# Kernel optimization log

Measured on AMD Instinct MI355X. Metric: run time of the kernel, lower is better.

## Reference

```python
import jax, jax.numpy as jnp
import numpy as np
import math

D = 1024      # d_model
H = 4096      # expert hidden
E = 8         # num_experts
K = 2         # top_k
CAP_FACTOR = 1.25
B, S = 4, 2048
T = B * S
CAP = int(math.ceil(CAP_FACTOR * T * K / E))  # 2560


def setup_inputs() -> dict:
    key = jax.random.key(0)
    ks = jax.random.split(key, 6)
    x  = jax.random.normal(ks[0], (B, S, D), dtype=jnp.float32)
    Wr = jax.random.normal(ks[1], (D, E), dtype=jnp.float32) * (1.0 / np.sqrt(D))
    W1 = jax.random.normal(ks[2], (E, D, H), dtype=jnp.float32) * (1.0 / np.sqrt(D))
    b1 = jnp.zeros((E, H), dtype=jnp.float32)
    W2 = jax.random.normal(ks[3], (E, H, D), dtype=jnp.float32) * (1.0 / np.sqrt(H))
    b2 = jnp.zeros((E, D), dtype=jnp.float32)
    return {"x": x, "Wr": Wr, "W1": W1, "b1": b1, "W2": W2, "b2": b2}


def reference(x, Wr, W1, b1, W2, b2):
    x_flat = x.reshape(T, D)

    # ---- Router: top-k softmax gating (temp = 1.0), renormalized weights ----
    logits = jnp.einsum('td,de->te', x_flat, Wr)
    probs = jax.nn.softmax(logits, axis=-1)
    topk_w, topk_idx = jax.lax.top_k(probs, K)            # [T,K]
    topk_w = topk_w / jnp.sum(topk_w, axis=-1, keepdims=True)

    # ---- Vectorized capacity-based dispatch ----
    e = topk_idx.reshape(-1)                               # [T*K] expert id per pair
    onehot = jax.nn.one_hot(e, E, dtype=jnp.int32)         # [T*K, E]
    pos_all = jnp.cumsum(onehot, axis=0) - 1               # slot within expert
    pos = jnp.take_along_axis(pos_all, e[:, None], axis=1)[:, 0]
    keep = pos < CAP
    # dropped pairs go to a dummy slot E*CAP (sliced off / zero-padded)
    dest = jnp.where(keep, e * CAP + pos, E * CAP)         # [T*K]

    x_pairs = jnp.repeat(x_flat, K, axis=0)                # [T*K, D]
    buf = jnp.zeros((E * CAP + 1, D), dtype=x.dtype).at[dest].set(x_pairs)
    expert_in = buf[:E * CAP].reshape(E, CAP, D)

    # ---- Grouped expert MLP (GELU) ----
    h = jax.nn.gelu(jnp.einsum('ecd,edh->ech', expert_in, W1) + b1[:, None, :])
    expert_out = jnp.einsum('ech,ehd->ecd', h, W2) + b2[:, None, :]

    # ---- Combine: gather back and weight; dropped tokens get zeros ----
    out_pad = jnp.concatenate(
        [expert_out.reshape(E * CAP, D), jnp.zeros((1, D), dtype=x.dtype)], axis=0)
    y_pairs = out_pad[dest] * topk_w.reshape(-1)[:, None]  # [T*K, D]
    y_flat = y_pairs.reshape(T, K, D).sum(axis=1)
    return y_flat.reshape(B, S, D)
```

## Files before the change

### kernel.cpp

```cpp
#include <hip/hip_runtime.h>
#include <stdint.h>

#define D_MODEL 1024
#define H_DIM   4096
#define NE      8
#define NCAP    2560
#define NTOK    8192
#define NPAIR   (NTOK * 2)

typedef __attribute__((ext_vector_type(8))) __bf16 bf16x8;
typedef __attribute__((ext_vector_type(4))) float  f32x4;
typedef __attribute__((ext_vector_type(8))) unsigned short ushort8;

__device__ __forceinline__ unsigned short f2bf(float f) {
  union { float f; unsigned u; } v; v.f = f;
  unsigned r = v.u + 0x7fffu + ((v.u >> 16) & 1u);
  return (unsigned short)(r >> 16);
}
__device__ __forceinline__ float bf2f(unsigned short s) {
  union { unsigned u; float f; } v; v.u = ((unsigned)s) << 16;
  return v.f;
}
__device__ __forceinline__ float gelu_tanh(float x) {
  float u = 0.7978845608028654f * (x + 0.044715f * x * x * x);
  float e = __expf(2.0f * u);
  float th = 1.0f - 2.0f / (e + 1.0f);
  return 0.5f * x * (1.0f + th);
}
__device__ __forceinline__ void load_lds16(const void* g, void* l) {
  __builtin_amdgcn_global_load_lds(
      (const __attribute__((address_space(1))) unsigned int*)g,
      (__attribute__((address_space(3))) unsigned int*)l, 16, 0, 0);
}

__global__ __launch_bounds__(256) void router_kernel(
    const float* __restrict__ x, const float* __restrict__ Wr,
    int* __restrict__ pair_e, float* __restrict__ pair_w) {
  int lane = threadIdx.x & 63;
  int t = blockIdx.x * 4 + (threadIdx.x >> 6);
  float acc[NE];
#pragma unroll
  for (int e = 0; e < NE; ++e) acc[e] = 0.0f;
  const float* xr = x + (size_t)t * D_MODEL;
  for (int d = lane; d < D_MODEL; d += 64) {
    float xv = xr[d];
#pragma unroll
    for (int e = 0; e < NE; ++e) acc[e] = fmaf(xv, Wr[d * NE + e], acc[e]);
  }
#pragma unroll
  for (int off = 32; off > 0; off >>= 1) {
#pragma unroll
    for (int e = 0; e < NE; ++e) acc[e] += __shfl_down(acc[e], off, 64);
  }
  if (lane == 0) {
    int i1 = 0;
#pragma unroll
    for (int e = 1; e < NE; ++e) if (acc[e] > acc[i1]) i1 = e;
    int i2 = (i1 == 0) ? 1 : 0;
#pragma unroll
    for (int e = 0; e < NE; ++e) if (e != i1 && acc[e] > acc[i2]) i2 = e;
    float p2 = expf(acc[i2] - acc[i1]);
    float inv = 1.0f / (1.0f + p2);
    pair_e[t * 2]     = i1;  pair_e[t * 2 + 1] = i2;
    pair_w[t * 2]     = inv;
    pair_w[t * 2 + 1] = p2 * inv;
  }
}

__global__ __launch_bounds__(1024) void assign_kernel(
    const int* __restrict__ pair_e, int* __restrict__ pair_dest,
    int* __restrict__ counts) {
  __shared__ int wtot[16][NE];
  const int tid = threadIdx.x;
  const int lane = tid & 63, w = tid >> 6;

  int ids[16];
  const int4* pe = (const int4*)(pair_e + tid * 16);
#pragma unroll
  for (int q = 0; q < 4; ++q) {
    int4 v = pe[q];
    ids[q * 4 + 0] = v.x; ids[q * 4 + 1] = v.y;
    ids[q * 4 + 2] = v.z; ids[q * 4 + 3] = v.w;
  }
  int c[NE];
#pragma unroll
  for (int e = 0; e < NE; ++e) c[e] = 0;
#pragma unroll
  for (int j = 0; j < 16; ++j) c[ids[j]]++;

  int incl[NE];
#pragma unroll
  for (int e = 0; e < NE; ++e) incl[e] = c[e];
#pragma unroll
  for (int d = 1; d < 64; d <<= 1) {
#pragma unroll
    for (int e = 0; e < NE; ++e) {
      int u = __shfl_up(incl[e], d, 64);
      if (lane >= d) incl[e] += u;
    }
  }
  if (lane == 63) {
#pragma unroll
    for (int e = 0; e < NE; ++e) wtot[w][e] = incl[e];
  }
  __syncthreads();
  if (tid < NE) {
    int run = 0;
#pragma unroll
    for (int ww = 0; ww < 16; ++ww) {
      int t2 = wtot[ww][tid];
      wtot[ww][tid] = run;
      run += t2;
    }
    counts[tid] = run < NCAP ? run : NCAP;
  }
  __syncthreads();

  int off[NE];
#pragma unroll
  for (int e = 0; e < NE; ++e) off[e] = wtot[w][e] + incl[e] - c[e];
#pragma unroll
  for (int j = 0; j < 16; ++j) {
    int e = ids[j];
    int pos = off[e]++;
    pair_dest[tid * 16 + j] = (pos < NCAP) ? (e * NCAP + pos) : (NE * NCAP);
  }
}

__global__ __launch_bounds__(64) void dispatch_kernel(
    const float* __restrict__ x, const int* __restrict__ pair_dest,
    unsigned short* __restrict__ Xd) {
  int i = blockIdx.x;
  int dest = pair_dest[i];
  if (dest >= NE * NCAP) return;
  int lane = threadIdx.x;
  int t = i >> 1;
  const float4* xr = (const float4*)(x + (size_t)t * D_MODEL);
  ushort4* dr = (ushort4*)(Xd + (size_t)dest * D_MODEL);
#pragma unroll
  for (int c = 0; c < 4; ++c) {
    float4 v = xr[lane + c * 64];
    ushort4 o;
    o.x = f2bf(v.x); o.y = f2bf(v.y); o.z = f2bf(v.z); o.w = f2bf(v.w);
    dr[lane + c * 64] = o;
  }
}

__global__ __launch_bounds__(256) void transpose_cvt(
    const float* __restrict__ src, unsigned short* __restrict__ dst,
    int R, int C) {
  __shared__ float tile[64][69];
  int e = blockIdx.z;
  int c0 = blockIdx.x * 64, r0 = blockIdx.y * 64;
  const float* s = src + (size_t)e * R * C + (size_t)r0 * C + c0;
  int tc = (threadIdx.x & 15) * 4;
  int tr = threadIdx.x >> 4;
#pragma unroll
  for (int it = 0; it < 4; ++it) {
    int row = tr + it * 16;
    float4 v = *(const float4*)(s + (size_t)row * C + tc);
    tile[row][tc]     = v.x; tile[row][tc + 1] = v.y;
    tile[row][tc + 2] = v.z; tile[row][tc + 3] = v.w;
  }
  __syncthreads();
  unsigned short* d = dst + (size_t)e * R * C + (size_t)c0 * R + r0;
  int oc  = threadIdx.x >> 3;
  int orr = (threadIdx.x & 7) * 8;
#pragma unroll
  for (int it = 0; it < 2; ++it) {
    int crow = oc + it * 32;
    ushort8 v;
#pragma unroll
    for (int j = 0; j < 8; ++j) v[j] = f2bf(tile[orr + j][crow]);
    *(ushort8*)(d + (size_t)crow * R + orr) = v;
  }
}

__global__ __launch_bounds__(512, 2) void moe_gemm_pipe(
    const unsigned short* __restrict__ Abase,
    const unsigned short* __restrict__ Bbase,
    const float* __restrict__ bias,
    unsigned short* __restrict__ Cout,
    const int* __restrict__ counts,
    int N, int K, int NX, int do_gelu) {
  const int M = NCAP;
  const int KT = K >> 6;
  __shared__ char smem[131072];

  int orig = blockIdx.x;
  int q = (NX * NE) >> 3;
  int wgid = (orig & 7) * q + (orig >> 3);
  const int e = wgid / NX;
  int r = wgid % NX;

  int grp = r >> 2, lid = r & 3;
  int gm = grp % 5, gn = grp / 5;
  const int m0 = (gm * 2 + (lid & 1)) * 256;
  const int n0 = (gn * 2 + (lid >> 1)) * 256;
  if (m0 >= counts[e]) return;

  const int tid = threadIdx.x;
  const int lane = tid & 63;
  const int wid = tid >> 6;
  const int wm = (wid >> 2) * 128;
  const int wn = (wid & 3) * 64;

  const unsigned short* A = Abase + (size_t)e * M * K;
  const unsigned short* B = Bbase + (size_t)e * N * K;

  f32x4 acc[8][4];
  f32x4 zero = {0.f, 0.f, 0.f, 0.f};
#pragma unroll
  for (int i = 0; i < 8; ++i)
#pragma unroll
    for (int j = 0; j < 4; ++j) acc[i][j] = zero;

  const unsigned short* ga[4];
  const unsigned short* gb[4];
  int ldso[4];
#pragma unroll
  for (int c = 0; c < 4; ++c) {
    int ci = c * 512 + tid;
    int row = ci >> 3;
    int sc = (ci & 7) ^ (row & 7);
    ga[c] = A + (size_t)(m0 + row) * K + sc * 8;
    gb[c] = B + (size_t)(n0 + row) * K + sc * 8;
    ldso[c] = (c * 512 + wid * 64) * 16;
  }

#pragma unroll
  for (int c = 0; c < 4; ++c) {
    load_lds16(ga[c], smem + ldso[c]);          ga[c] += 64;
    load_lds16(gb[c], smem + 32768 + ldso[c]);  gb[c] += 64;
  }

  for (int kt = 0; kt < KT; ++kt) {
    __syncthreads();
    const char* Ab = smem + (kt & 1) * 65536;
    const char* Bb = Ab + 32768;
    if (kt + 1 < KT) {
      char* An = smem + ((kt + 1) & 1) * 65536;
#pragma unroll
      for (int c = 0; c < 4; ++c) {
        load_lds16(ga[c], An + ldso[c]);          ga[c] += 64;
        load_lds16(gb[c], An + 32768 + ldso[c]);  gb[c] += 64;
      }
    }
    {
      bf16x8 af[8], bfr[4];
      int lc = (lane >> 4);
#pragma unroll
      for (int f = 0; f < 8; ++f) {
        int ar = wm + f * 16 + (lane & 15);
        af[f] = *(const bf16x8*)(Ab + ar * 128 + ((lc ^ (ar & 7)) * 16));
      }
#pragma unroll
      for (int f = 0; f < 4; ++f) {
        int br = wn + f * 16 + (lane & 15);
        bfr[f] = *(const bf16x8*)(Bb + br * 128 + ((lc ^ (br & 7)) * 16));
      }
      __builtin_amdgcn_s_setprio(1);
#pragma unroll
      for (int i = 0; i < 8; ++i)
#pragma unroll
        for (int j = 0; j < 4; ++j)
          acc[i][j] = __builtin_amdgcn_mfma_f32_16x16x32_bf16(
              af[i], bfr[j], acc[i][j], 0, 0, 0);
      __builtin_amdgcn_s_setprio(0);
    }
    __builtin_amdgcn_s_barrier();
    {
      bf16x8 af[8], bfr[4];
      int lc = 4 + (lane >> 4);
#pragma unroll
      for (int f = 0; f < 8; ++f) {
        int ar = wm + f * 16 + (lane & 15);
        af[f] = *(const bf16x8*)(Ab + ar * 128 + ((lc ^ (ar & 7)) * 16));
      }
#pragma unroll
      for (int f = 0; f < 4; ++f) {
        int br = wn + f * 16 + (lane & 15);
        bfr[f] = *(const bf16x8*)(Bb + br * 128 + ((lc ^ (br & 7)) * 16));
      }
      __builtin_amdgcn_s_setprio(1);
#pragma unroll
      for (int i = 0; i < 8; ++i)
#pragma unroll
        for (int j = 0; j < 4; ++j)
          acc[i][j] = __builtin_amdgcn_mfma_f32_16x16x32_bf16(
              af[i], bfr[j], acc[i][j], 0, 0, 0);
      __builtin_amdgcn_s_setprio(0);
    }
  }

  __syncthreads();
  const float* be = bias + (size_t)e * N;
#pragma unroll
  for (int i = 0; i < 8; ++i) {
    int rbase = wm + i * 16 + ((lane >> 4) << 2);
#pragma unroll
    for (int j = 0; j < 4; ++j) {
      int col = wn + j * 16 + (lane & 15);
      float bv = be[n0 + col];
#pragma unroll
      for (int r2 = 0; r2 < 4; ++r2) {
        float xv = acc[i][j][r2] + bv;
        if (do_gelu) xv = gelu_tanh(xv);
        *(unsigned short*)(smem + (size_t)(rbase + r2) * 512 + col * 2) = f2bf(xv);
      }
    }
  }
  __syncthreads();
#pragma unroll
  for (int it = 0; it < 16; ++it) {
    int idx = it * 4096 + tid * 8;
    int row = idx >> 8, col = idx & 255;
    ushort8 v = *(const ushort8*)(smem + (size_t)idx * 2);
    *(ushort8*)(Cout + ((size_t)e * M + m0 + row) * N + n0 + col) = v;
  }
}

__global__ __launch_bounds__(256) void combine_kernel(
    const unsigned short* __restrict__ Ebuf,
    const int* __restrict__ pair_dest,
    const float* __restrict__ pair_w,
    float* __restrict__ out) {
  int t = blockIdx.x;
  int d0 = threadIdx.x * 4;
  float4 r = {0.f, 0.f, 0.f, 0.f};
#pragma unroll
  for (int k = 0; k < 2; ++k) {
    int dest = pair_dest[t * 2 + k];
    if (dest < NE * NCAP) {
      float w = pair_w[t * 2 + k];
      ushort4 v = *(const ushort4*)(Ebuf + (size_t)dest * D_MODEL + d0);
      r.x += w * bf2f(v.x); r.y += w * bf2f(v.y);
      r.z += w * bf2f(v.z); r.w += w * bf2f(v.w);
    }
  }
  *(float4*)(out + (size_t)t * D_MODEL + d0) = r;
}

extern "C" void kernel_launch(void* const* d_in, const int* in_sizes, int n_in,
                              void* d_out, int out_size, void* d_ws, size_t ws_size,
                              hipStream_t stream) {
  const float* x  = (const float*)d_in[0];
  const float* Wr = (const float*)d_in[1];
  const float* W1 = (const float*)d_in[2];
  const float* b1 = (const float*)d_in[3];
  const float* W2 = (const float*)d_in[4];
  const float* b2 = (const float*)d_in[5];
  float* out = (float*)d_out;

  char* ws = (char*)d_ws;
  unsigned short* W1T  = (unsigned short*)(ws + 0);
  unsigned short* W2T  = (unsigned short*)(ws + 67108864);
  unsigned short* Xd   = (unsigned short*)(ws + 134217728);
  unsigned short* Ebuf = Xd;
  unsigned short* Hbuf = (unsigned short*)(ws + 176160768);
  int*   pair_e    = (int*)(ws + 343932928);
  float* pair_w    = (float*)(ws + 343998464);
  int*   pair_dest = (int*)(ws + 344064000);
  int*   counts    = (int*)(ws + 344129536);

  transpose_cvt<<<dim3(H_DIM / 64, D_MODEL / 64, NE), 256, 0, stream>>>(W1, W1T, D_MODEL, H_DIM);
  transpose_cvt<<<dim3(D_MODEL / 64, H_DIM / 64, NE), 256, 0, stream>>>(W2, W2T, H_DIM, D_MODEL);

  router_kernel<<<NTOK / 4, 256, 0, stream>>>(x, Wr, pair_e, pair_w);
  assign_kernel<<<1, 1024, 0, stream>>>(pair_e, pair_dest, counts);
  dispatch_kernel<<<NPAIR, 64, 0, stream>>>(x, pair_dest, Xd);

  {
    int nx = (NCAP / 256) * (H_DIM / 256);
    moe_gemm_pipe<<<nx * NE, 512, 0, stream>>>(
        Xd, W1T, b1, Hbuf, counts, H_DIM, D_MODEL, nx, 1);
  }
  {
    int nx = (NCAP / 256) * (D_MODEL / 256);
    moe_gemm_pipe<<<nx * NE, 512, 0, stream>>>(
        Hbuf, W2T, b2, Ebuf, counts, D_MODEL, H_DIM, nx, 0);
  }

  combine_kernel<<<NTOK, 256, 0, stream>>>(Ebuf, pair_dest, pair_w, out);
}
```

Measured before the change: 807.3 us.

## Switch expert GEMM to 4-stage K=32 LDS pipeline with explicit vmcnt waits

Restructures the main GEMM loop from a double-buffered K=64 tile into a four-slot ring of K=32 tiles, keeping three tiles of global-to-LDS loads in flight. Each iteration uses a manual s_waitcnt vmcnt count and a single barrier instead of __syncthreads plus two half-steps. A new XOR swizzle fits the 64-byte LDS rows. The goal is deeper latency hiding of global loads, at the cost of twice as many barriers per K and reliance on exact vmcnt accounting.

```diff
diff --git a/kernel.cpp b/kernel.cpp
--- a/kernel.cpp
+++ b/kernel.cpp
@@ -184,7 +184,7 @@
     const int* __restrict__ counts,
     int N, int K, int NX, int do_gelu) {
   const int M = NCAP;
-  const int KT = K >> 6;
+  const int KT = K >> 5;
   __shared__ char smem[131072];
 
   int orig = blockIdx.x;
@@ -215,83 +215,69 @@
 #pragma unroll
     for (int j = 0; j < 4; ++j) acc[i][j] = zero;
 
-  const unsigned short* ga[4];
-  const unsigned short* gb[4];
-  int ldso[4];
-#pragma unroll
-  for (int c = 0; c < 4; ++c) {
+  const unsigned short* ga[2];
+  const unsigned short* gb[2];
+  int ldsoA[2], ldsoB[2];
+#pragma unroll
+  for (int c = 0; c < 2; ++c) {
     int ci = c * 512 + tid;
-    int row = ci >> 3;
-    int sc = (ci & 7) ^ (row & 7);
-    ga[c] = A + (size_t)(m0 + row) * K + sc * 8;
-    gb[c] = B + (size_t)(n0 + row) * K + sc * 8;
-    ldso[c] = (c * 512 + wid * 64) * 16;
-  }
-
-#pragma unroll
-  for (int c = 0; c < 4; ++c) {
-    load_lds16(ga[c], smem + ldso[c]);          ga[c] += 64;
-    load_lds16(gb[c], smem + 32768 + ldso[c]);  gb[c] += 64;
-  }
+    int row = ci >> 2;
+    int gch = (ci & 3) ^ ((row >> 1) & 3);
+    ga[c] = A + (size_t)(m0 + row) * K + gch * 8;
+    gb[c] = B + (size_t)(n0 + row) * K + gch * 8;
+    ldsoA[c] = (c * 512 + wid * 64) * 16;
+    ldsoB[c] = 16384 + (c * 512 + wid * 64) * 16;
+  }
+
+#define STAGE_TILE(slot)                                        \
+  {                                                             \
+    char* Sb = smem + (slot) * 32768;                           \
+    _Pragma("unroll")                                           \
+    for (int c = 0; c < 2; ++c) {                               \
+      load_lds16(ga[c], Sb + ldsoA[c]);  ga[c] += 32;           \
+      load_lds16(gb[c], Sb + ldsoB[c]);  gb[c] += 32;           \
+    }                                                           \
+  }
+
+  STAGE_TILE(0)
+  STAGE_TILE(1)
+  STAGE_TILE(2)
 
   for (int kt = 0; kt < KT; ++kt) {
-    __syncthreads();
-    const char* Ab = smem + (kt & 1) * 65536;
-    const char* Bb = Ab + 32768;
-    if (kt + 1 < KT) {
-      char* An = smem + ((kt + 1) & 1) * 65536;
-#pragma unroll
-      for (int c = 0; c < 4; ++c) {
-        load_lds16(ga[c], An + ldso[c]);          ga[c] += 64;
-        load_lds16(gb[c], An + 32768 + ldso[c]);  gb[c] += 64;
-      }
-    }
-    {
-      bf16x8 af[8], bfr[4];
-      int lc = (lane >> 4);
-#pragma unroll
-      for (int f = 0; f < 8; ++f) {
-        int ar = wm + f * 16 + (lane & 15);
-        af[f] = *(const bf16x8*)(Ab + ar * 128 + ((lc ^ (ar & 7)) * 16));
-      }
-#pragma unroll
-      for (int f = 0; f < 4; ++f) {
-        int br = wn + f * 16 + (lane & 15);
-        bfr[f] = *(const bf16x8*)(Bb + br * 128 + ((lc ^ (br & 7)) * 16));
-      }
-      __builtin_amdgcn_s_setprio(1);
-#pragma unroll
-      for (int i = 0; i < 8; ++i)
-#pragma unroll
-        for (int j = 0; j < 4; ++j)
-          acc[i][j] = __builtin_amdgcn_mfma_f32_16x16x32_bf16(
-              af[i], bfr[j], acc[i][j], 0, 0, 0);
-      __builtin_amdgcn_s_setprio(0);
-    }
+    int rem = KT - 1 - kt;
+    if (rem >= 2)      { asm volatile("s_waitcnt vmcnt(8)" ::: "memory"); }
+    else if (rem == 1) { asm volatile("s_waitcnt vmcnt(4)" ::: "memory"); }
+    else               { asm volatile("s_waitcnt vmcnt(0)" ::: "memory"); }
+    __builtin_amdgcn_sched_barrier(0);
     __builtin_amdgcn_s_barrier();
-    {
-      bf16x8 af[8], bfr[4];
-      int lc = 4 + (lane >> 4);
-#pragma unroll
-      for (int f = 0; f < 8; ++f) {
-        int ar = wm + f * 16 + (lane & 15);
-        af[f] = *(const bf16x8*)(Ab + ar * 128 + ((lc ^ (ar & 7)) * 16));
-      }
-#pragma unroll
-      for (int f = 0; f < 4; ++f) {
-        int br = wn + f * 16 + (lane & 15);
-        bfr[f] = *(const bf16x8*)(Bb + br * 128 + ((lc ^ (br & 7)) * 16));
-      }
-      __builtin_amdgcn_s_setprio(1);
-#pragma unroll
-      for (int i = 0; i < 8; ++i)
-#pragma unroll
-        for (int j = 0; j < 4; ++j)
-          acc[i][j] = __builtin_amdgcn_mfma_f32_16x16x32_bf16(
-              af[i], bfr[j], acc[i][j], 0, 0, 0);
-      __builtin_amdgcn_s_setprio(0);
-    }
-  }
+    __builtin_amdgcn_sched_barrier(0);
+
+    if (kt + 3 < KT) STAGE_TILE((kt + 3) & 3)
+
+    const char* Ab = smem + (size_t)(kt & 3) * 32768;
+    const char* Bb = Ab + 16384;
+    bf16x8 af[8], bfr[4];
+    int lc = lane >> 4;
+#pragma unroll
+    for (int f = 0; f < 8; ++f) {
+      int ar = wm + f * 16 + (lane & 15);
+      af[f] = *(const bf16x8*)(Ab + ar * 64 + ((lc ^ ((ar >> 1) & 3)) * 16));
+    }
+#pragma unroll
+    for (int f = 0; f < 4; ++f) {
+      int br = wn + f * 16 + (lane & 15);
+      bfr[f] = *(const bf16x8*)(Bb + br * 64 + ((lc ^ ((br >> 1) & 3)) * 16));
+    }
+    __builtin_amdgcn_s_setprio(1);
+#pragma unroll
+    for (int i = 0; i < 8; ++i)
+#pragma unroll
+      for (int j = 0; j < 4; ++j)
+        acc[i][j] = __builtin_amdgcn_mfma_f32_16x16x32_bf16(
+            af[i], bfr[j], acc[i][j], 0, 0, 0);
+    __builtin_amdgcn_s_setprio(0);
+  }
+#undef STAGE_TILE
 
   __syncthreads();
   const float* be = bias + (size_t)e * N;
```

Measured after the change: 819.5 us. No clear change (+1.5%).
